# Kernel optimization log

Measured on AMD Instinct MI355X. Metric: run time of the kernel, lower is better.

The kernel has to match this reference:

```python
import jax, jax.numpy as jnp
import numpy as np

ANGLE_NUM = 8500
EMBED_LEN = 32
B, N = 4, 8500


def _conv1d(x, w, b):
    # x: [B, C, N], w: [O, I, K]
    y = jax.lax.conv_general_dilated(x, w, window_strides=(1,), padding='SAME',
                                     dimension_numbers=('NCH', 'OIH', 'NCH'))
    return y + b[None, :, None]


def setup_inputs() -> dict:
    key = jax.random.key(0)
    k = jax.random.split(key, 8)
    intensity = jax.random.uniform(k[0], (B, N), dtype=jnp.float32) * 100.0
    angle = jax.random.randint(k[1], (B, N), 0, ANGLE_NUM, dtype=jnp.int32)
    embed_table = jax.random.normal(k[2], (ANGLE_NUM, EMBED_LEN), dtype=jnp.float32)
    s = 1.0 / np.sqrt(EMBED_LEN * 3)
    w1 = jax.random.normal(k[3], (EMBED_LEN, EMBED_LEN, 3), dtype=jnp.float32) * s
    b1 = jnp.zeros((EMBED_LEN,), dtype=jnp.float32)
    w2 = jax.random.normal(k[4], (EMBED_LEN, EMBED_LEN, 3), dtype=jnp.float32) * s
    b2 = jnp.zeros((EMBED_LEN,), dtype=jnp.float32)
    return {"intensity": intensity, "angle": angle, "embed_table": embed_table,
            "w1": w1, "b1": b1, "w2": w2, "b2": b2}


def reference(intensity, angle, embed_table, w1, b1, w2, b2):
    b = intensity.shape[0]
    a = angle.reshape(b, -1)                      # [B, N] int
    inten = intensity.reshape(b, -1, 1) / 100.0   # [B, N, 1]
    # rank-1 outer product -> [B, N, N] scores, row softmax
    scores = inten @ jnp.transpose(inten, (0, 2, 1))
    atten = jax.nn.softmax(scores, axis=-1)
    x = embed_table[a]                            # [B, N, E] embedding lookup
    x = atten @ x                                 # [B, N, E]
    x = jnp.transpose(x, (0, 2, 1))               # [B, E, N]
    # residual TCN block: conv-relu-conv + skip, relu
    h = jax.nn.relu(_conv1d(x, w1, b1))
    h = _conv1d(h, w2, b2)
    return jax.nn.relu(x + h)
```

## Files before the change

### kernel.cpp

```cpp
#include <hip/hip_runtime.h>

#define NPOS 8500
#define BB 4
#define EMB 32
#define KP 16
#define MOM 528
#define NBLK 64
#define JPB 133
#define JPS 17
#define TOUT 133
#define NT 64
#define STG 137
#define STR 138
#define THR 576

__device__ __constant__ float c_invf[KP] = {
    1.f, 1.f, 0.5f, 1.f/6.f, 1.f/24.f, 1.f/120.f, 1.f/720.f, 1.f/5040.f,
    1.f/40320.f, 1.f/362880.f, 1.f/3628800.f, 1.f/39916800.f,
    1.f/479001600.f, 1.f/6227020800.f, 1.f/87178291200.f, 1.f/1307674368000.f};

__global__ __launch_bounds__(256) void moments_partial(
    const float* __restrict__ inten, const int* __restrict__ angle,
    const float* __restrict__ emb, float* __restrict__ part,
    const float* __restrict__ w1, const float* __restrict__ w2,
    float* __restrict__ wt)
{
    if (blockIdx.x == BB * NBLK) {
        for (int i = threadIdx.x; i < 3072; i += 256) {
            wt[i] = w1[(i & 31) * 96 + (i >> 5)];
            wt[3072 + i] = w2[(i & 31) * 96 + (i >> 5)];
        }
        return;
    }
    const int b = blockIdx.x >> 6;
    const int blk = blockIdx.x & 63;
    const int t = threadIdx.x;
    const int sub = t >> 5;
    const int e = t & 31;
    const int jlo = blk * JPB;
    const int jhi = min(jlo + JPB, NPOS);
    const int js = jlo + sub * JPS;
    const int je = min(js + JPS, jhi);

    float accM[KP], accS[KP];
#pragma unroll
    for (int k = 0; k < KP; ++k) { accM[k] = 0.f; accS[k] = 0.f; }

    const float* ib = inten + b * NPOS;
    const int* ab = angle + b * NPOS;
    for (int j = js; j < je; ++j) {
        const float v = ib[j] * 0.01f;
        const int a = ab[j];
        const float ev = emb[a * EMB + e];
        float p = 1.0f;
        accM[0] += ev;
        accS[0] += 1.0f;
#pragma unroll
        for (int k = 1; k < KP; ++k) {
            p *= v;
            accM[k] = fmaf(p, ev, accM[k]);
            accS[k] += p;
        }
    }

    __shared__ float red[8][MOM];
#pragma unroll
    for (int k = 0; k < KP; ++k) red[sub][KP + k * EMB + e] = accM[k];
    if (e == 0) {
#pragma unroll
        for (int k = 0; k < KP; ++k) red[sub][k] = accS[k];
    }
    __syncthreads();
    for (int i = t; i < MOM; i += 256) {
        float s = 0.f;
#pragma unroll
        for (int u = 0; u < 8; ++u) s += red[u][i];
        part[((size_t)b * MOM + i) * NBLK + blk] = s;
    }
}

__global__ __launch_bounds__(THR) void main_kernel(
    const float* __restrict__ inten, const float* __restrict__ part,
    const float* __restrict__ wt, const float* __restrict__ b1,
    const float* __restrict__ b2, float* __restrict__ out)
{
    __shared__ float moms[MOM];
    __shared__ float b1s[EMB], b2s[EMB];
    __shared__ float xs[EMB][STR];
    __shared__ float hs[EMB][STR];

    const int t = threadIdx.x;
    const int b = blockIdx.x >> 6;
    const int tile = blockIdx.x & 63;
    const int start = tile * TOUT;
    const int e = t & 31;

    if (t < EMB) { b1s[t] = b1[t]; b2s[t] = b2[t]; }
    if (t < MOM) {
        const float4* pr = (const float4*)&part[((size_t)b * MOM + t) * NBLK];
        float4 a0 = pr[0], a1 = pr[1], a2 = pr[2], a3 = pr[3];
#pragma unroll
        for (int u = 4; u < 16; u += 4) {
            const float4 v0 = pr[u], v1 = pr[u + 1], v2 = pr[u + 2], v3 = pr[u + 3];
            a0.x += v0.x; a0.y += v0.y; a0.z += v0.z; a0.w += v0.w;
            a1.x += v1.x; a1.y += v1.y; a1.z += v1.z; a1.w += v1.w;
            a2.x += v2.x; a2.y += v2.y; a2.z += v2.z; a2.w += v2.w;
            a3.x += v3.x; a3.y += v3.y; a3.z += v3.z; a3.w += v3.w;
        }
        const float s = ((a0.x + a0.y) + (a0.z + a0.w)) + ((a1.x + a1.y) + (a1.z + a1.w))
                      + ((a2.x + a2.y) + (a2.z + a2.w)) + ((a3.x + a3.y) + (a3.z + a3.w));
        const int k = (t < KP) ? t : ((t - KP) >> 5);
        moms[t] = s * c_invf[k];
    }
    __syncthreads();

    float Mreg[KP], Sreg[KP];
#pragma unroll
    for (int k = 0; k < KP; ++k) {
        Mreg[k] = moms[KP + k * EMB + e];
        Sreg[k] = moms[k];
    }

    for (int i = t; i < STG * EMB; i += THR) {
        const int pos = i >> 5;
        const int gp = start - 2 + pos;
        const bool valid = (gp >= 0) && (gp < NPOS);
        const float u = valid ? inten[b * NPOS + gp] * 0.01f : 0.f;
        float num = Mreg[KP - 1], den = Sreg[KP - 1];
#pragma unroll
        for (int k = KP - 2; k >= 0; --k) {
            num = fmaf(num, u, Mreg[k]);
            den = fmaf(den, u, Sreg[k]);
        }
        const float rd = valid ? __builtin_amdgcn_rcpf(den) : 0.f;
        xs[e][pos] = num * rd;
    }
    __syncthreads();

    const int wv = t >> 6;
    const int lane = t & 63;

    if (wv < 8) {
        const int o0 = __builtin_amdgcn_readfirstlane(wv << 2);
        const int i0 = 2 * lane;
        float a[4][2];
#pragma unroll
        for (int oo = 0; oo < 4; ++oo) { a[oo][0] = b1s[o0 + oo]; a[oo][1] = b1s[o0 + oo]; }
        const float* wp = wt + o0;
#pragma unroll 4
        for (int c = 0; c < 32; ++c) {
            const float2 xa = *(const float2*)&xs[c][i0];
            const float2 xb = *(const float2*)&xs[c][i0 + 2];
            const float* wr = wp + c * 96;
#pragma unroll
            for (int oo = 0; oo < 4; ++oo) {
                const float wA = wr[oo], wB = wr[32 + oo], wC = wr[64 + oo];
                a[oo][0] = fmaf(wA, xa.x, fmaf(wB, xa.y, fmaf(wC, xb.x, a[oo][0])));
                a[oo][1] = fmaf(wA, xa.y, fmaf(wB, xb.x, fmaf(wC, xb.y, a[oo][1])));
            }
        }
        const int gp0 = start - 1 + i0;
        const bool v0 = (gp0 >= 0) && (gp0 < NPOS);
        const bool v1 = (gp0 + 1 >= 0) && (gp0 + 1 < NPOS);
#pragma unroll
        for (int oo = 0; oo < 4; ++oo) {
            float2 hv;
            hv.x = v0 ? fmaxf(a[oo][0], 0.f) : 0.f;
            hv.y = v1 ? fmaxf(a[oo][1], 0.f) : 0.f;
            *(float2*)&hs[o0 + oo][i0] = hv;
        }
    } else {
        const int g2 = lane >> 3, p = lane & 7;
        if (p < 7) {
            const int o0e = g2 << 2;
            const int j = 129 + p;
            float a[4];
#pragma unroll
            for (int oo = 0; oo < 4; ++oo) a[oo] = b1s[o0e + oo];
#pragma unroll 4
            for (int c = 0; c < 32; ++c) {
                const float x0 = xs[c][j - 1], x1 = xs[c][j], x2 = xs[c][j + 1];
                const float4 W0 = *(const float4*)&wt[(c * 3 + 0) * 32 + o0e];
                const float4 W1 = *(const float4*)&wt[(c * 3 + 1) * 32 + o0e];
                const float4 W2 = *(const float4*)&wt[(c * 3 + 2) * 32 + o0e];
                const float wa[4] = {W0.x, W0.y, W0.z, W0.w};
                const float wb[4] = {W1.x, W1.y, W1.z, W1.w};
                const float wc[4] = {W2.x, W2.y, W2.z, W2.w};
#pragma unroll
                for (int oo = 0; oo < 4; ++oo)
                    a[oo] = fmaf(wa[oo], x0, fmaf(wb[oo], x1, fmaf(wc[oo], x2, a[oo])));
            }
            const int gp = start - 2 + j;
            const bool v = gp < NPOS;
#pragma unroll
            for (int oo = 0; oo < 4; ++oo)
                hs[o0e + oo][j - 1] = v ? fmaxf(a[oo], 0.f) : 0.f;
        }
    }
    __syncthreads();

    if (wv < 8) {
        const int o0 = __builtin_amdgcn_readfirstlane(wv << 2);
        const int i0 = 2 * lane;
        float a[4][2];
#pragma unroll
        for (int oo = 0; oo < 4; ++oo) { a[oo][0] = b2s[o0 + oo]; a[oo][1] = b2s[o0 + oo]; }
        const float* wp = wt + 3072 + o0;
#pragma unroll 4
        for (int c = 0; c < 32; ++c) {
            const float2 ha = *(const float2*)&hs[c][i0];
            const float2 hb = *(const float2*)&hs[c][i0 + 2];
            const float* wr = wp + c * 96;
#pragma unroll
            for (int oo = 0; oo < 4; ++oo) {
                const float wA = wr[oo], wB = wr[32 + oo], wC = wr[64 + oo];
                a[oo][0] = fmaf(wA, ha.x, fmaf(wB, ha.y, fmaf(wC, hb.x, a[oo][0])));
                a[oo][1] = fmaf(wA, ha.y, fmaf(wB, hb.x, fmaf(wC, hb.y, a[oo][1])));
            }
        }
        const int p0 = start + i0;
        if (p0 < NPOS) {
            const bool full = (p0 + 1 < NPOS);
#pragma unroll
            for (int oo = 0; oo < 4; ++oo) {
                const float2 xr = *(const float2*)&xs[o0 + oo][i0 + 2];
                const float r0 = fmaxf(xr.x + a[oo][0], 0.f);
                const float r1 = fmaxf(xr.y + a[oo][1], 0.f);
                float* ob = out + (size_t)(b * EMB + o0 + oo) * NPOS + p0;
                if (full) *(float2*)ob = make_float2(r0, r1);
                else ob[0] = r0;
            }
        }
    } else {
        const int g2 = lane >> 3, p = lane & 7;
        if (p < 5) {
            const int o0e = g2 << 2;
            const int q = 130 + p;
            float a[4];
#pragma unroll
            for (int oo = 0; oo < 4; ++oo) a[oo] = b2s[o0e + oo];
#pragma unroll 4
            for (int c = 0; c < 32; ++c) {
                const float h0 = hs[c][q - 2], h1 = hs[c][q - 1], h2 = hs[c][q];
                const float4 W0 = *(const float4*)&wt[3072 + (c * 3 + 0) * 32 + o0e];
                const float4 W1 = *(const float4*)&wt[3072 + (c * 3 + 1) * 32 + o0e];
                const float4 W2 = *(const float4*)&wt[3072 + (c * 3 + 2) * 32 + o0e];
                const float wa[4] = {W0.x, W0.y, W0.z, W0.w};
                const float wb[4] = {W1.x, W1.y, W1.z, W1.w};
                const float wc[4] = {W2.x, W2.y, W2.z, W2.w};
#pragma unroll
                for (int oo = 0; oo < 4; ++oo)
                    a[oo] = fmaf(wa[oo], h0, fmaf(wb[oo], h1, fmaf(wc[oo], h2, a[oo])));
            }
            const int pos = start + q - 2;
            if (pos < NPOS) {
#pragma unroll
                for (int oo = 0; oo < 4; ++oo) {
                    const float r = fmaxf(xs[o0e + oo][q] + a[oo], 0.f);
                    out[(size_t)(b * EMB + o0e + oo) * NPOS + pos] = r;
                }
            }
        }
    }
}

extern "C" void kernel_launch(void* const* d_in, const int* in_sizes, int n_in,
                              void* d_out, int out_size, void* d_ws, size_t ws_size,
                              hipStream_t stream) {
    const float* inten = (const float*)d_in[0];
    const int* angle = (const int*)d_in[1];
    const float* emb = (const float*)d_in[2];
    const float* w1 = (const float*)d_in[3];
    const float* b1 = (const float*)d_in[4];
    const float* w2 = (const float*)d_in[5];
    const float* b2 = (const float*)d_in[6];
    float* out = (float*)d_out;

    float* part = (float*)d_ws;
    float* wt = (float*)((char*)d_ws + (size_t)BB * MOM * NBLK * 4);

    moments_partial<<<BB * NBLK + 1, 256, 0, stream>>>(inten, angle, emb, part, w1, w2, wt);
    main_kernel<<<BB * NT, THR, 0, stream>>>(inten, part, wt, b1, b2, out);
}
```

Before: 27.41 us.

## Double moments-kernel threads, use power tree, drop weight transpose, prefetch intensities

The moments kernel now runs 512 threads per block with half as many positions per 32-lane group. Each thread processes two positions per iteration and builds powers with a multiplication tree, and the two half-waves are combined with a cross-lane shuffle before the shared-memory reduction. The extra block that transposed the conv weights is removed, so the main kernel reads w1/w2 and the biases straight from global memory with wave-uniform indices. The main kernel also issues its intensity loads before the moment reduction to hide their latency, at the cost of more registers and less coalesced weight access.

```diff
diff --git a/kernel.cpp b/kernel.cpp
--- a/kernel.cpp
+++ b/kernel.cpp
@@ -7,7 +7,7 @@
 #define MOM 528
 #define NBLK 64
 #define JPB 133
-#define JPS 17
+#define JPS 9
 #define TOUT 133
 #define NT 64
 #define STG 137
@@ -19,19 +19,21 @@
     1.f/40320.f, 1.f/362880.f, 1.f/3628800.f, 1.f/39916800.f,
     1.f/479001600.f, 1.f/6227020800.f, 1.f/87178291200.f, 1.f/1307674368000.f};
 
-__global__ __launch_bounds__(256) void moments_partial(
+__device__ __forceinline__ void powtree(float v, float* p) {
+    const float v2 = v * v;
+    const float v4 = v2 * v2;
+    const float v8 = v4 * v4;
+    p[1] = v;          p[2] = v2;         p[3] = v2 * v;
+    p[4] = v4;         p[5] = v4 * v;     p[6] = v4 * v2;
+    p[7] = v4 * p[3];  p[8] = v8;         p[9] = v8 * v;
+    p[10] = v8 * v2;   p[11] = v8 * p[3]; p[12] = v8 * v4;
+    p[13] = v8 * p[5]; p[14] = v8 * p[6]; p[15] = v8 * p[7];
+}
+
+__global__ __launch_bounds__(512) void moments_partial(
     const float* __restrict__ inten, const int* __restrict__ angle,
-    const float* __restrict__ emb, float* __restrict__ part,
-    const float* __restrict__ w1, const float* __restrict__ w2,
-    float* __restrict__ wt)
+    const float* __restrict__ emb, float* __restrict__ part)
 {
-    if (blockIdx.x == BB * NBLK) {
-        for (int i = threadIdx.x; i < 3072; i += 256) {
-            wt[i] = w1[(i & 31) * 96 + (i >> 5)];
-            wt[3072 + i] = w2[(i & 31) * 96 + (i >> 5)];
-        }
-        return;
-    }
     const int b = blockIdx.x >> 6;
     const int blk = blockIdx.x & 63;
     const int t = threadIdx.x;
@@ -48,30 +50,55 @@
 
     const float* ib = inten + b * NPOS;
     const int* ab = angle + b * NPOS;
-    for (int j = js; j < je; ++j) {
+    int j = js;
+    for (; j + 1 < je; j += 2) {
+        const float va = ib[j] * 0.01f;
+        const float vb = ib[j + 1] * 0.01f;
+        const float eva = emb[ab[j] * EMB + e];
+        const float evb = emb[ab[j + 1] * EMB + e];
+        float pa[KP], pb[KP];
+        powtree(va, pa);
+        powtree(vb, pb);
+        accM[0] += eva + evb;
+        accS[0] += 2.0f;
+#pragma unroll
+        for (int k = 1; k < KP; ++k) {
+            accM[k] = fmaf(pa[k], eva, accM[k]);
+            accM[k] = fmaf(pb[k], evb, accM[k]);
+            accS[k] += pa[k] + pb[k];
+        }
+    }
+    if (j < je) {
         const float v = ib[j] * 0.01f;
-        const int a = ab[j];
-        const float ev = emb[a * EMB + e];
-        float p = 1.0f;
+        const float ev = emb[ab[j] * EMB + e];
+        float p[KP];
+        powtree(v, p);
         accM[0] += ev;
         accS[0] += 1.0f;
 #pragma unroll
         for (int k = 1; k < KP; ++k) {
-            p *= v;
-            accM[k] = fmaf(p, ev, accM[k]);
-            accS[k] += p;
-        }
-    }
-
+            accM[k] = fmaf(p[k], ev, accM[k]);
+            accS[k] += p[k];
+        }
+    }
+
+#pragma unroll
+    for (int k = 0; k < KP; ++k) {
+        accM[k] += __shfl_xor(accM[k], 32);
+        accS[k] += __shfl_xor(accS[k], 32);
+    }
     __shared__ float red[8][MOM];
-#pragma unroll
-    for (int k = 0; k < KP; ++k) red[sub][KP + k * EMB + e] = accM[k];
-    if (e == 0) {
-#pragma unroll
-        for (int k = 0; k < KP; ++k) red[sub][k] = accS[k];
+    const int wv = t >> 6;
+    if ((t & 32) == 0) {
+#pragma unroll
+        for (int k = 0; k < KP; ++k) red[wv][KP + k * EMB + e] = accM[k];
+        if (e == 0) {
+#pragma unroll
+            for (int k = 0; k < KP; ++k) red[wv][k] = accS[k];
+        }
     }
     __syncthreads();
-    for (int i = t; i < MOM; i += 256) {
+    for (int i = t; i < MOM; i += 512) {
         float s = 0.f;
 #pragma unroll
         for (int u = 0; u < 8; ++u) s += red[u][i];
@@ -81,11 +108,11 @@
 
 __global__ __launch_bounds__(THR) void main_kernel(
     const float* __restrict__ inten, const float* __restrict__ part,
-    const float* __restrict__ wt, const float* __restrict__ b1,
-    const float* __restrict__ b2, float* __restrict__ out)
+    const float* __restrict__ w1, const float* __restrict__ b1,
+    const float* __restrict__ w2, const float* __restrict__ b2,
+    float* __restrict__ out)
 {
     __shared__ float moms[MOM];
-    __shared__ float b1s[EMB], b2s[EMB];
     __shared__ float xs[EMB][STR];
     __shared__ float hs[EMB][STR];
 
@@ -95,7 +122,19 @@
     const int start = tile * TOUT;
     const int e = t & 31;
 
-    if (t < EMB) { b1s[t] = b1[t]; b2s[t] = b2[t]; }
+    float uu[8];
+#pragma unroll
+    for (int q = 0; q < 8; ++q) {
+        const int i = t + q * THR;
+        float u = -1.0f;
+        if (i < STG * EMB) {
+            const int pos = i >> 5;
+            const int gp = start - 2 + pos;
+            if (gp >= 0 && gp < NPOS) u = inten[b * NPOS + gp] * 0.01f;
+        }
+        uu[q] = u;
+    }
+
     if (t < MOM) {
         const float4* pr = (const float4*)&part[((size_t)b * MOM + t) * NBLK];
         float4 a0 = pr[0], a1 = pr[1], a2 = pr[2], a3 = pr[3];
@@ -121,19 +160,23 @@
         Sreg[k] = moms[k];
     }
 
-    for (int i = t; i < STG * EMB; i += THR) {
-        const int pos = i >> 5;
-        const int gp = start - 2 + pos;
-        const bool valid = (gp >= 0) && (gp < NPOS);
-        const float u = valid ? inten[b * NPOS + gp] * 0.01f : 0.f;
-        float num = Mreg[KP - 1], den = Sreg[KP - 1];
-#pragma unroll
-        for (int k = KP - 2; k >= 0; --k) {
-            num = fmaf(num, u, Mreg[k]);
-            den = fmaf(den, u, Sreg[k]);
-        }
-        const float rd = valid ? __builtin_amdgcn_rcpf(den) : 0.f;
-        xs[e][pos] = num * rd;
+#pragma unroll
+    for (int q = 0; q < 8; ++q) {
+        const int i = t + q * THR;
+        if (i < STG * EMB) {
+            const int pos = i >> 5;
+            const float u = uu[q];
+            const bool valid = (u >= 0.f);
+            const float uc = valid ? u : 0.f;
+            float num = Mreg[KP - 1], den = Sreg[KP - 1];
+#pragma unroll
+            for (int k = KP - 2; k >= 0; --k) {
+                num = fmaf(num, uc, Mreg[k]);
+                den = fmaf(den, uc, Sreg[k]);
+            }
+            const float rd = valid ? __builtin_amdgcn_rcpf(den) : 0.f;
+            xs[e][pos] = num * rd;
+        }
     }
     __syncthreads();
 
@@ -143,18 +186,19 @@
     if (wv < 8) {
         const int o0 = __builtin_amdgcn_readfirstlane(wv << 2);
         const int i0 = 2 * lane;
+        const float* W = w1 + o0 * 96;
         float a[4][2];
 #pragma unroll
-        for (int oo = 0; oo < 4; ++oo) { a[oo][0] = b1s[o0 + oo]; a[oo][1] = b1s[o0 + oo]; }
-        const float* wp = wt + o0;
+        for (int oo = 0; oo < 4; ++oo) { const float bv = b1[o0 + oo]; a[oo][0] = bv; a[oo][1] = bv; }
 #pragma unroll 4
         for (int c = 0; c < 32; ++c) {
             const float2 xa = *(const float2*)&xs[c][i0];
             const float2 xb = *(const float2*)&xs[c][i0 + 2];
-            const float* wr = wp + c * 96;
 #pragma unroll
             for (int oo = 0; oo < 4; ++oo) {
-                const float wA = wr[oo], wB = wr[32 + oo], wC = wr[64 + oo];
+                const float wA = W[oo * 96 + c * 3 + 0];
+                const float wB = W[oo * 96 + c * 3 + 1];
+                const float wC = W[oo * 96 + c * 3 + 2];
                 a[oo][0] = fmaf(wA, xa.x, fmaf(wB, xa.y, fmaf(wC, xb.x, a[oo][0])));
                 a[oo][1] = fmaf(wA, xa.y, fmaf(wB, xb.x, fmaf(wC, xb.y, a[oo][1])));
             }
@@ -176,19 +220,17 @@
             const int j = 129 + p;
             float a[4];
 #pragma unroll
-            for (int oo = 0; oo < 4; ++oo) a[oo] = b1s[o0e + oo];
+            for (int oo = 0; oo < 4; ++oo) a[oo] = b1[o0e + oo];
 #pragma unroll 4
             for (int c = 0; c < 32; ++c) {
                 const float x0 = xs[c][j - 1], x1 = xs[c][j], x2 = xs[c][j + 1];
-                const float4 W0 = *(const float4*)&wt[(c * 3 + 0) * 32 + o0e];
-                const float4 W1 = *(const float4*)&wt[(c * 3 + 1) * 32 + o0e];
-                const float4 W2 = *(const float4*)&wt[(c * 3 + 2) * 32 + o0e];
-                const float wa[4] = {W0.x, W0.y, W0.z, W0.w};
-                const float wb[4] = {W1.x, W1.y, W1.z, W1.w};
-                const float wc[4] = {W2.x, W2.y, W2.z, W2.w};
-#pragma unroll
-                for (int oo = 0; oo < 4; ++oo)
-                    a[oo] = fmaf(wa[oo], x0, fmaf(wb[oo], x1, fmaf(wc[oo], x2, a[oo])));
+#pragma unroll
+                for (int oo = 0; oo < 4; ++oo) {
+                    const float wa = w1[(o0e + oo) * 96 + c * 3 + 0];
+                    const float wb = w1[(o0e + oo) * 96 + c * 3 + 1];
+                    const float wc = w1[(o0e + oo) * 96 + c * 3 + 2];
+                    a[oo] = fmaf(wa, x0, fmaf(wb, x1, fmaf(wc, x2, a[oo])));
+                }
             }
             const int gp = start - 2 + j;
             const bool v = gp < NPOS;
@@ -202,18 +244,19 @@
     if (wv < 8) {
         const int o0 = __builtin_amdgcn_readfirstlane(wv << 2);
         const int i0 = 2 * lane;
+        const float* W = w2 + o0 * 96;
         float a[4][2];
 #pragma unroll
-        for (int oo = 0; oo < 4; ++oo) { a[oo][0] = b2s[o0 + oo]; a[oo][1] = b2s[o0 + oo]; }
-        const float* wp = wt + 3072 + o0;
+        for (int oo = 0; oo < 4; ++oo) { const float bv = b2[o0 + oo]; a[oo][0] = bv; a[oo][1] = bv; }
 #pragma unroll 4
         for (int c = 0; c < 32; ++c) {
             const float2 ha = *(const float2*)&hs[c][i0];
             const float2 hb = *(const float2*)&hs[c][i0 + 2];
-            const float* wr = wp + c * 96;
 #pragma unroll
             for (int oo = 0; oo < 4; ++oo) {
-                const float wA = wr[oo], wB = wr[32 + oo], wC = wr[64 + oo];
+                const float wA = W[oo * 96 + c * 3 + 0];
+                const float wB = W[oo * 96 + c * 3 + 1];
+                const float wC = W[oo * 96 + c * 3 + 2];
                 a[oo][0] = fmaf(wA, ha.x, fmaf(wB, ha.y, fmaf(wC, hb.x, a[oo][0])));
                 a[oo][1] = fmaf(wA, ha.y, fmaf(wB, hb.x, fmaf(wC, hb.y, a[oo][1])));
             }
@@ -238,19 +281,17 @@
             const int q = 130 + p;
             float a[4];
 #pragma unroll
-            for (int oo = 0; oo < 4; ++oo) a[oo] = b2s[o0e + oo];
+            for (int oo = 0; oo < 4; ++oo) a[oo] = b2[o0e + oo];
 #pragma unroll 4
             for (int c = 0; c < 32; ++c) {
                 const float h0 = hs[c][q - 2], h1 = hs[c][q - 1], h2 = hs[c][q];
-                const float4 W0 = *(const float4*)&wt[3072 + (c * 3 + 0) * 32 + o0e];
-                const float4 W1 = *(const float4*)&wt[3072 + (c * 3 + 1) * 32 + o0e];
-                const float4 W2 = *(const float4*)&wt[3072 + (c * 3 + 2) * 32 + o0e];
-                const float wa[4] = {W0.x, W0.y, W0.z, W0.w};
-                const float wb[4] = {W1.x, W1.y, W1.z, W1.w};
-                const float wc[4] = {W2.x, W2.y, W2.z, W2.w};
-#pragma unroll
-                for (int oo = 0; oo < 4; ++oo)
-                    a[oo] = fmaf(wa[oo], h0, fmaf(wb[oo], h1, fmaf(wc[oo], h2, a[oo])));
+#pragma unroll
+                for (int oo = 0; oo < 4; ++oo) {
+                    const float wa = w2[(o0e + oo) * 96 + c * 3 + 0];
+                    const float wb = w2[(o0e + oo) * 96 + c * 3 + 1];
+                    const float wc = w2[(o0e + oo) * 96 + c * 3 + 2];
+                    a[oo] = fmaf(wa, h0, fmaf(wb, h1, fmaf(wc, h2, a[oo])));
+                }
             }
             const int pos = start + q - 2;
             if (pos < NPOS) {
@@ -277,8 +318,7 @@
     float* out = (float*)d_out;
 
     float* part = (float*)d_ws;
-    float* wt = (float*)((char*)d_ws + (size_t)BB * MOM * NBLK * 4);
-
-    moments_partial<<<BB * NBLK + 1, 256, 0, stream>>>(inten, angle, emb, part, w1, w2, wt);
-    main_kernel<<<BB * NT, THR, 0, stream>>>(inten, part, wt, b1, b2, out);
+
+    moments_partial<<<BB * NBLK, 512, 0, stream>>>(inten, angle, emb, part);
+    main_kernel<<<BB * NT, THR, 0, stream>>>(inten, part, w1, b1, w2, b2, out);
 }
```

After: 26.90 us. No clear change (-1.9%).
